# Optimization experiments

Measured on AMD Instinct MI355X. Metric: run time of the kernel, lower is better.

Reference implementation:

```python
import jax, jax.numpy as jnp
import numpy as np

N_HEAD = 32
HEAD_DIM = 32  # must equal N_HEAD due to the module's einsum index reuse
N_EMBD = N_HEAD * HEAD_DIM
VOCAB = 32000
B, T = 2, 64
TEMP_MIN = 0.1


def setup_inputs() -> dict:
    key = jax.random.key(0)
    ks = jax.random.split(key, 8)
    inv = 1.0 / np.sqrt(HEAD_DIM)
    return {
        "x": jax.random.normal(ks[0], (B, T, N_EMBD), dtype=jnp.float32),
        "vocab_emb": jax.random.normal(ks[1], (VOCAB, N_EMBD), dtype=jnp.float32) * 0.02,
        "W_ffn": jax.random.normal(ks[2], (HEAD_DIM, HEAD_DIM), dtype=jnp.float32) * inv,
        "b_ffn": jnp.zeros((HEAD_DIM,), dtype=jnp.float32),
        "temps": jnp.ones((N_HEAD,), dtype=jnp.float32),
        "W_ref": jax.random.normal(ks[3], (HEAD_DIM, HEAD_DIM), dtype=jnp.float32) * inv,
        "b_ref": jnp.zeros((HEAD_DIM,), dtype=jnp.float32),
        "W_gate": jax.random.normal(ks[4], (HEAD_DIM, HEAD_DIM), dtype=jnp.float32) * inv,
        "b_gate": jnp.zeros((HEAD_DIM,), dtype=jnp.float32),
    }


def reference(x, vocab_emb, W_ffn, b_ffn, temps, W_ref, b_ref, W_gate, b_gate):
    Bs, Ts, C = x.shape
    # per-head channel decomposition: (B*T, n_head, head_dim)
    xc = x.reshape(Bs * Ts, N_HEAD, HEAD_DIM)
    # channel_ffns: shared Linear over the head_dim axis (torch Linear: x @ W.T + b)
    ffn = jnp.einsum('bnh,dh->bnd', xc, W_ffn) + b_ffn
    # vocab channels: (n_head, vocab, head_dim)
    vc = vocab_emb.reshape(VOCAB, N_HEAD, HEAD_DIM).transpose(1, 0, 2)
    temps_c = jnp.clip(temps, TEMP_MIN, None)[None, :, None]

    def vocab_project(q):
        # faithful to torch: einsum('bnh,hvd->bnv') contracts q's head_dim
        # against vc's HEAD axis and sums over d as well (requires head_dim == n_head)
        logits = jnp.einsum('bnh,hvd->bnv', q, vc)
        w = jax.nn.softmax(logits / temps_c, axis=-1)  # (B*T, n_head, vocab)
        return jnp.einsum('bnv,hvd->bnh', w, vc)

    vocab_out = vocab_project(ffn)  # (B*T, n_head, head_dim)

    # refinement stage (use_vocab_refinement=True)
    refinement = jnp.tanh(jnp.einsum('bnh,dh->bnd', xc, W_ref) + b_ref)
    gate = jax.nn.sigmoid(jnp.einsum('bnh,dh->bnd', xc, W_gate) + b_gate)
    refined = vocab_out * (1.0 - gate) + refinement * gate
    vocab_out = vocab_project(refined)

    # dropout p=0 (eval) -> identity
    return vocab_out.reshape(Bs, Ts, C)
```

## Files before the change

kernel.cpp:

```cpp
#include <hip/hip_runtime.h>
#include <hip/hip_bf16.h>
#include <cstdint>

typedef unsigned int uint;
typedef unsigned short ushort_t;

typedef __attribute__((ext_vector_type(8))) short short8;
typedef __attribute__((ext_vector_type(4))) short short4_t;
typedef __attribute__((ext_vector_type(4))) float float4_t;

#define NEMBD 1024
#define VOCAB 32000
#define LOG2E 1.4426950408889634f

__device__ __forceinline__ ushort_t f2bf_rne(float f) {
    uint u = __float_as_uint(f);
    u += 0x7fffu + ((u >> 16) & 1u);
    return (ushort_t)(u >> 16);
}

__global__ void k_build_st(const float* __restrict__ ve, ushort_t* __restrict__ ST) {
    int v = blockIdx.x;
    int t = threadIdx.x;
    const float4* row = (const float4*)(ve + (size_t)v * NEMBD);
    float4 f = row[t];
    float s = f.x + f.y + f.z + f.w;
    s += __shfl_down(s, 4, 8);
    s += __shfl_down(s, 2, 8);
    s += __shfl_down(s, 1, 8);
    if ((t & 7) == 0) ST[v * 32 + (t >> 3)] = f2bf_rne(s);
}

__global__ void k_pack(const ushort_t* __restrict__ ST, ushort_t* __restrict__ SA,
                       ushort_t* __restrict__ S2) {
    int c = blockIdx.x;
    int t = threadIdx.x;
    if (t < 128) {
        int tile = t >> 6, lane = t & 63;
        int quad = lane >> 4, lo = lane & 15;
        uint4 d = *(const uint4*)(ST + ((size_t)(c * 32 + tile * 16 + lo)) * 32 + quad * 8);
        ((uint4*)SA)[c * 128 + t] = d;
    } else {
        int tt = t - 128;
        int f = tt >> 6, l = tt & 63;
        int quad = l >> 4, lo = l & 15;
        uint w[4];
        #pragma unroll
        for (int t2 = 0; t2 < 2; t2++) {
            #pragma unroll
            for (int jj = 0; jj < 2; jj++) {
                ushort_t v0 = ST[(c * 32 + t2 * 16 + quad * 4 + jj * 2 + 0) * 32 + f * 16 + lo];
                ushort_t v1 = ST[(c * 32 + t2 * 16 + quad * 4 + jj * 2 + 1) * 32 + f * 16 + lo];
                w[t2 * 2 + jj] = (uint)v0 | ((uint)v1 << 16);
            }
        }
        ((uint4*)S2)[c * 128 + tt] = make_uint4(w[0], w[1], w[2], w[3]);
    }
}

__global__ void k_q1(const float* __restrict__ x, const float* __restrict__ W,
                     const float* __restrict__ b, const float* __restrict__ temps,
                     ushort_t* __restrict__ q1) {
    int tid = blockIdx.x * 256 + threadIdx.x;
    int i = tid >> 5, d = tid & 31, n = i & 31;
    const float* xr = x + i * 32;
    float s = b[d];
    #pragma unroll
    for (int h = 0; h < 32; h++) s += xr[h] * W[d * 32 + h];
    q1[tid] = f2bf_rne(s * (LOG2E / fmaxf(temps[n], 0.1f)));
}

__launch_bounds__(256, 4)
__global__ void k_proj(const ushort_t* __restrict__ SA, const ushort_t* __restrict__ S2,
                       const ushort_t* __restrict__ q, float* __restrict__ pN,
                       float* __restrict__ pD) {
    int g = blockIdx.x >> 4, p = blockIdx.x & 15;
    int w = threadIdx.x >> 6, lane = threadIdx.x & 63;
    int quad = lane >> 4, lo = lane & 15;

    short8 qf[4];
    #pragma unroll
    for (int s = 0; s < 4; s++)
        qf[s] = *(const short8*)(q + ((g * 64 + s * 16 + lo) * 32 + quad * 8));

    float4_t pv0[4], pv1[4];
    float dsum[4];
    #pragma unroll
    for (int s = 0; s < 4; s++) {
        pv0[s] = (float4_t){0.f, 0.f, 0.f, 0.f};
        pv1[s] = (float4_t){0.f, 0.f, 0.f, 0.f};
        dsum[s] = 0.f;
    }
    const float4_t zero4 = (float4_t){0.f, 0.f, 0.f, 0.f};

    int start = (p * 125) >> 1, end = ((p + 1) * 125) >> 1;
    int k = start + w;
    const ushort_t* pa = SA + (size_t)k * 1024 + lane * 8;
    const ushort_t* pb = S2 + (size_t)k * 1024 + lane * 8;
    short8 a0n = *(const short8*)pa;
    short8 a1n = *(const short8*)(pa + 512);
    short8 b0n = *(const short8*)pb;
    short8 b1n = *(const short8*)(pb + 512);

    while (true) {
        short8 a0 = a0n, a1 = a1n, s0 = b0n, s1 = b1n;
        k += 4;
        bool more = (k < end);
        if (more) {
            pa += 4096; pb += 4096;
            a0n = *(const short8*)pa;
            a1n = *(const short8*)(pa + 512);
            b0n = *(const short8*)pb;
            b1n = *(const short8*)(pb + 512);
        }
        short4_t b00 = {s0[0], s0[1], s0[2], s0[3]};
        short4_t b01 = {s0[4], s0[5], s0[6], s0[7]};
        short4_t b10 = {s1[0], s1[1], s1[2], s1[3]};
        short4_t b11 = {s1[4], s1[5], s1[6], s1[7]};

        #pragma unroll
        for (int s = 0; s < 4; s++) {
            float4_t l0 = __builtin_amdgcn_mfma_f32_16x16x32_bf16(a0, qf[s], zero4, 0, 0, 0);
            float4_t l1 = __builtin_amdgcn_mfma_f32_16x16x32_bf16(a1, qf[s], zero4, 0, 0, 0);
            float e0 = __builtin_amdgcn_exp2f(l0[0]);
            float e1 = __builtin_amdgcn_exp2f(l0[1]);
            float e2 = __builtin_amdgcn_exp2f(l0[2]);
            float e3 = __builtin_amdgcn_exp2f(l0[3]);
            float f0 = __builtin_amdgcn_exp2f(l1[0]);
            float f1 = __builtin_amdgcn_exp2f(l1[1]);
            float f2 = __builtin_amdgcn_exp2f(l1[2]);
            float f3 = __builtin_amdgcn_exp2f(l1[3]);
            uint u0 = __builtin_amdgcn_perm(__float_as_uint(e1), __float_as_uint(e0), 0x07060302u);
            uint u1 = __builtin_amdgcn_perm(__float_as_uint(e3), __float_as_uint(e2), 0x07060302u);
            uint u2 = __builtin_amdgcn_perm(__float_as_uint(f1), __float_as_uint(f0), 0x07060302u);
            uint u3 = __builtin_amdgcn_perm(__float_as_uint(f3), __float_as_uint(f2), 0x07060302u);
            dsum[s] += __uint_as_float(u0 << 16) + __uint_as_float(u0 & 0xffff0000u)
                     + __uint_as_float(u1 << 16) + __uint_as_float(u1 & 0xffff0000u)
                     + __uint_as_float(u2 << 16) + __uint_as_float(u2 & 0xffff0000u)
                     + __uint_as_float(u3 << 16) + __uint_as_float(u3 & 0xffff0000u);
            union { uint u[2]; short4_t s4; } c0u, c1u;
            c0u.u[0] = u0; c0u.u[1] = u1;
            c1u.u[0] = u2; c1u.u[1] = u3;
            short4_t P0 = c0u.s4, P1 = c1u.s4;
            pv0[s] = __builtin_amdgcn_mfma_f32_16x16x16bf16_1k(P0, b00, pv0[s], 0, 0, 0);
            pv0[s] = __builtin_amdgcn_mfma_f32_16x16x16bf16_1k(P1, b01, pv0[s], 0, 0, 0);
            pv1[s] = __builtin_amdgcn_mfma_f32_16x16x16bf16_1k(P0, b10, pv1[s], 0, 0, 0);
            pv1[s] = __builtin_amdgcn_mfma_f32_16x16x16bf16_1k(P1, b11, pv1[s], 0, 0, 0);
        }
        if (!more) break;
    }

    #pragma unroll
    for (int s = 0; s < 4; s++) {
        dsum[s] += __shfl_xor(dsum[s], 16, 64);
        dsum[s] += __shfl_xor(dsum[s], 32, 64);
    }

    __shared__ float red[4][64][9];
    int gp = blockIdx.x;
    for (int s = 0; s < 4; s++) {
        #pragma unroll
        for (int r = 0; r < 4; r++) {
            red[w][lane][r]     = pv0[s][r];
            red[w][lane][4 + r] = pv1[s][r];
        }
        red[w][lane][8] = dsum[s];
        __syncthreads();
        if (w == 0) {
            #pragma unroll
            for (int r = 0; r < 4; r++) {
                float n0 = 0.f, n1 = 0.f;
                #pragma unroll
                for (int wv = 0; wv < 4; wv++) {
                    n0 += red[wv][lane][r];
                    n1 += red[wv][lane][4 + r];
                }
                int ql = s * 16 + quad * 4 + r;
                pN[((size_t)gp * 64 + ql) * 32 + lo]      = n0;
                pN[((size_t)gp * 64 + ql) * 32 + 16 + lo] = n1;
            }
            if (quad == 0) {
                float dd = red[0][lane][8] + red[1][lane][8]
                         + red[2][lane][8] + red[3][lane][8];
                pD[gp * 64 + s * 16 + lo] = dd;
            }
        }
        __syncthreads();
    }
}

__global__ void k_refine(const float* __restrict__ pN, const float* __restrict__ pD,
                         const float* __restrict__ x,
                         const float* __restrict__ Wr, const float* __restrict__ br,
                         const float* __restrict__ Wg, const float* __restrict__ bg,
                         const float* __restrict__ temps, ushort_t* __restrict__ q2) {
    int tid = blockIdx.x * 256 + threadIdx.x;
    int i = tid >> 5, h = tid & 31, n = i & 31;
    int g = i >> 6, ql = i & 63;
    float N = 0.f, D = 0.f;
    #pragma unroll
    for (int p = 0; p < 16; p++) {
        N += pN[((size_t)(g * 16 + p) * 64 + ql) * 32 + h];
        D += pD[(g * 16 + p) * 64 + ql];
    }
    float vo = N / D;
    const float* xr = x + i * 32;
    float sr = br[h], sg = bg[h];
    #pragma unroll
    for (int h2 = 0; h2 < 32; h2++) {
        sr += xr[h2] * Wr[h * 32 + h2];
        sg += xr[h2] * Wg[h * 32 + h2];
    }
    float ref  = tanhf(sr);
    float gate = 1.f / (1.f + __expf(-sg));
    float refined = vo * (1.f - gate) + ref * gate;
    q2[tid] = f2bf_rne(refined * (LOG2E / fmaxf(temps[n], 0.1f)));
}

__global__ void k_final(const float* __restrict__ pN, const float* __restrict__ pD,
                        float* __restrict__ out) {
    int tid = blockIdx.x * 256 + threadIdx.x;
    int i = tid >> 5, h = tid & 31;
    int g = i >> 6, ql = i & 63;
    float N = 0.f, D = 0.f;
    #pragma unroll
    for (int p = 0; p < 16; p++) {
        N += pN[((size_t)(g * 16 + p) * 64 + ql) * 32 + h];
        D += pD[(g * 16 + p) * 64 + ql];
    }
    out[tid] = N / D;
}

extern "C" void kernel_launch(void* const* d_in, const int* in_sizes, int n_in,
                              void* d_out, int out_size, void* d_ws, size_t ws_size,
                              hipStream_t stream) {
    const float* x     = (const float*)d_in[0];
    const float* ve    = (const float*)d_in[1];
    const float* Wf    = (const float*)d_in[2];
    const float* bfn   = (const float*)d_in[3];
    const float* temps = (const float*)d_in[4];
    const float* Wr    = (const float*)d_in[5];
    const float* br    = (const float*)d_in[6];
    const float* Wg    = (const float*)d_in[7];
    const float* bg    = (const float*)d_in[8];
    float* out = (float*)d_out;

    char* ws = (char*)d_ws;
    ushort_t* ST = (ushort_t*)ws;
    ushort_t* SA = (ushort_t*)(ws + 2048000);
    ushort_t* S2 = (ushort_t*)(ws + 4096000);
    ushort_t* q1 = (ushort_t*)(ws + 6144000);
    ushort_t* q2 = (ushort_t*)(ws + 6144000 + 262144);
    char* base = ws + 6144000 + 2 * 262144;
    float* pNa = (float*)base;
    float* pDa = (float*)(base + 8388608);
    float* pNb = (float*)(base + 8388608 + 262144);
    float* pDb = (float*)(base + 2 * 8388608 + 262144);

    k_build_st<<<dim3(VOCAB), dim3(256), 0, stream>>>(ve, ST);
    k_pack<<<dim3(1000), dim3(256), 0, stream>>>(ST, SA, S2);
    k_q1<<<dim3(512), dim3(256), 0, stream>>>(x, Wf, bfn, temps, q1);
    k_proj<<<dim3(1024), dim3(256), 0, stream>>>(SA, S2, q1, pNa, pDa);
    k_refine<<<dim3(512), dim3(256), 0, stream>>>(pNa, pDa, x, Wr, br, Wg, bg, temps, q2);
    k_proj<<<dim3(1024), dim3(256), 0, stream>>>(SA, S2, q2, pNb, pDb);
    k_final<<<dim3(512), dim3(256), 0, stream>>>(pNb, pDb, out);
}
```

Measured before the change: 271.4 us.

## Compute softmax denominators via MFMA with ones and double-buffer chunk loads

The per-lane scalar denominator sum (bf16 unpacking, adds, and cross-lane shuffles) is replaced by two extra MFMAs per step that multiply the packed probabilities by a vector of ones, so row sums land in accumulator registers. The load loop is restructured into an explicit two-buffer ping-pong, issuing the next chunk's global loads before computing the current one. This cuts VALU work and shuffles in the hot loop but adds MFMA work and more live registers. The shared-memory reduction now also sums the extra accumulator.

```diff
diff --git a/kernel.cpp b/kernel.cpp
--- a/kernel.cpp
+++ b/kernel.cpp
@@ -70,6 +70,41 @@
     q1[tid] = f2bf_rne(s * (LOG2E / fmaxf(temps[n], 0.1f)));
 }
 
+#define CHUNK_COMPUTE(A0, A1, S0, S1)                                              \
+    {                                                                              \
+        short4_t b00 = {(S0)[0], (S0)[1], (S0)[2], (S0)[3]};                       \
+        short4_t b01 = {(S0)[4], (S0)[5], (S0)[6], (S0)[7]};                       \
+        short4_t b10 = {(S1)[0], (S1)[1], (S1)[2], (S1)[3]};                       \
+        short4_t b11 = {(S1)[4], (S1)[5], (S1)[6], (S1)[7]};                       \
+        _Pragma("unroll")                                                          \
+        for (int s = 0; s < 4; s++) {                                              \
+            float4_t l0 = __builtin_amdgcn_mfma_f32_16x16x32_bf16(A0, qf[s], zero4, 0, 0, 0); \
+            float4_t l1 = __builtin_amdgcn_mfma_f32_16x16x32_bf16(A1, qf[s], zero4, 0, 0, 0); \
+            float e0 = __builtin_amdgcn_exp2f(l0[0]);                              \
+            float e1 = __builtin_amdgcn_exp2f(l0[1]);                              \
+            float e2 = __builtin_amdgcn_exp2f(l0[2]);                              \
+            float e3 = __builtin_amdgcn_exp2f(l0[3]);                              \
+            float f0 = __builtin_amdgcn_exp2f(l1[0]);                              \
+            float f1 = __builtin_amdgcn_exp2f(l1[1]);                              \
+            float f2 = __builtin_amdgcn_exp2f(l1[2]);                              \
+            float f3 = __builtin_amdgcn_exp2f(l1[3]);                              \
+            uint u0 = __builtin_amdgcn_perm(__float_as_uint(e1), __float_as_uint(e0), 0x07060302u); \
+            uint u1 = __builtin_amdgcn_perm(__float_as_uint(e3), __float_as_uint(e2), 0x07060302u); \
+            uint u2 = __builtin_amdgcn_perm(__float_as_uint(f1), __float_as_uint(f0), 0x07060302u); \
+            uint u3 = __builtin_amdgcn_perm(__float_as_uint(f3), __float_as_uint(f2), 0x07060302u); \
+            union { uint u[2]; short4_t s4; } c0u, c1u;                            \
+            c0u.u[0] = u0; c0u.u[1] = u1;                                          \
+            c1u.u[0] = u2; c1u.u[1] = u3;                                          \
+            short4_t P0 = c0u.s4, P1 = c1u.s4;                                     \
+            pv0[s] = __builtin_amdgcn_mfma_f32_16x16x16bf16_1k(P0, b00, pv0[s], 0, 0, 0); \
+            pv0[s] = __builtin_amdgcn_mfma_f32_16x16x16bf16_1k(P1, b01, pv0[s], 0, 0, 0); \
+            pv1[s] = __builtin_amdgcn_mfma_f32_16x16x16bf16_1k(P0, b10, pv1[s], 0, 0, 0); \
+            pv1[s] = __builtin_amdgcn_mfma_f32_16x16x16bf16_1k(P1, b11, pv1[s], 0, 0, 0); \
+            dq[s]  = __builtin_amdgcn_mfma_f32_16x16x16bf16_1k(P0, ones, dq[s], 0, 0, 0);  \
+            dq[s]  = __builtin_amdgcn_mfma_f32_16x16x16bf16_1k(P1, ones, dq[s], 0, 0, 0);  \
+        }                                                                          \
+    }
+
 __launch_bounds__(256, 4)
 __global__ void k_proj(const ushort_t* __restrict__ SA, const ushort_t* __restrict__ S2,
                        const ushort_t* __restrict__ q, float* __restrict__ pN,
@@ -83,106 +118,65 @@
     for (int s = 0; s < 4; s++)
         qf[s] = *(const short8*)(q + ((g * 64 + s * 16 + lo) * 32 + quad * 8));
 
-    float4_t pv0[4], pv1[4];
-    float dsum[4];
+    float4_t pv0[4], pv1[4], dq[4];
     #pragma unroll
     for (int s = 0; s < 4; s++) {
         pv0[s] = (float4_t){0.f, 0.f, 0.f, 0.f};
         pv1[s] = (float4_t){0.f, 0.f, 0.f, 0.f};
-        dsum[s] = 0.f;
+        dq[s]  = (float4_t){0.f, 0.f, 0.f, 0.f};
     }
     const float4_t zero4 = (float4_t){0.f, 0.f, 0.f, 0.f};
+    const short4_t ones = {(short)0x3F80, (short)0x3F80, (short)0x3F80, (short)0x3F80};
 
     int start = (p * 125) >> 1, end = ((p + 1) * 125) >> 1;
-    int k = start + w;
-    const ushort_t* pa = SA + (size_t)k * 1024 + lane * 8;
-    const ushort_t* pb = S2 + (size_t)k * 1024 + lane * 8;
-    short8 a0n = *(const short8*)pa;
-    short8 a1n = *(const short8*)(pa + 512);
-    short8 b0n = *(const short8*)pb;
-    short8 b1n = *(const short8*)(pb + 512);
-
+    int base_k = start + w;
+    int cnt = (end - base_k + 3) >> 2;
+    const ushort_t* pa = SA + (size_t)base_k * 1024 + lane * 8;
+    const ushort_t* pb = S2 + (size_t)base_k * 1024 + lane * 8;
+
+    short8 a0A = *(const short8*)pa, a1A = *(const short8*)(pa + 512);
+    short8 s0A = *(const short8*)pb, s1A = *(const short8*)(pb + 512);
+    pa += 4096; pb += 4096;
+    short8 a0B, a1B, s0B, s1B;
+
+    int i = 0;
     while (true) {
-        short8 a0 = a0n, a1 = a1n, s0 = b0n, s1 = b1n;
-        k += 4;
-        bool more = (k < end);
-        if (more) {
-            pa += 4096; pb += 4096;
-            a0n = *(const short8*)pa;
-            a1n = *(const short8*)(pa + 512);
-            b0n = *(const short8*)pb;
-            b1n = *(const short8*)(pb + 512);
-        }
-        short4_t b00 = {s0[0], s0[1], s0[2], s0[3]};
-        short4_t b01 = {s0[4], s0[5], s0[6], s0[7]};
-        short4_t b10 = {s1[0], s1[1], s1[2], s1[3]};
-        short4_t b11 = {s1[4], s1[5], s1[6], s1[7]};
-
-        #pragma unroll
-        for (int s = 0; s < 4; s++) {
-            float4_t l0 = __builtin_amdgcn_mfma_f32_16x16x32_bf16(a0, qf[s], zero4, 0, 0, 0);
-            float4_t l1 = __builtin_amdgcn_mfma_f32_16x16x32_bf16(a1, qf[s], zero4, 0, 0, 0);
-            float e0 = __builtin_amdgcn_exp2f(l0[0]);
-            float e1 = __builtin_amdgcn_exp2f(l0[1]);
-            float e2 = __builtin_amdgcn_exp2f(l0[2]);
-            float e3 = __builtin_amdgcn_exp2f(l0[3]);
-            float f0 = __builtin_amdgcn_exp2f(l1[0]);
-            float f1 = __builtin_amdgcn_exp2f(l1[1]);
-            float f2 = __builtin_amdgcn_exp2f(l1[2]);
-            float f3 = __builtin_amdgcn_exp2f(l1[3]);
-            uint u0 = __builtin_amdgcn_perm(__float_as_uint(e1), __float_as_uint(e0), 0x07060302u);
-            uint u1 = __builtin_amdgcn_perm(__float_as_uint(e3), __float_as_uint(e2), 0x07060302u);
-            uint u2 = __builtin_amdgcn_perm(__float_as_uint(f1), __float_as_uint(f0), 0x07060302u);
-            uint u3 = __builtin_amdgcn_perm(__float_as_uint(f3), __float_as_uint(f2), 0x07060302u);
-            dsum[s] += __uint_as_float(u0 << 16) + __uint_as_float(u0 & 0xffff0000u)
-                     + __uint_as_float(u1 << 16) + __uint_as_float(u1 & 0xffff0000u)
-                     + __uint_as_float(u2 << 16) + __uint_as_float(u2 & 0xffff0000u)
-                     + __uint_as_float(u3 << 16) + __uint_as_float(u3 & 0xffff0000u);
-            union { uint u[2]; short4_t s4; } c0u, c1u;
-            c0u.u[0] = u0; c0u.u[1] = u1;
-            c1u.u[0] = u2; c1u.u[1] = u3;
-            short4_t P0 = c0u.s4, P1 = c1u.s4;
-            pv0[s] = __builtin_amdgcn_mfma_f32_16x16x16bf16_1k(P0, b00, pv0[s], 0, 0, 0);
-            pv0[s] = __builtin_amdgcn_mfma_f32_16x16x16bf16_1k(P1, b01, pv0[s], 0, 0, 0);
-            pv1[s] = __builtin_amdgcn_mfma_f32_16x16x16bf16_1k(P0, b10, pv1[s], 0, 0, 0);
-            pv1[s] = __builtin_amdgcn_mfma_f32_16x16x16bf16_1k(P1, b11, pv1[s], 0, 0, 0);
-        }
-        if (!more) break;
-    }
-
-    #pragma unroll
-    for (int s = 0; s < 4; s++) {
-        dsum[s] += __shfl_xor(dsum[s], 16, 64);
-        dsum[s] += __shfl_xor(dsum[s], 32, 64);
-    }
-
-    __shared__ float red[4][64][9];
+        a0B = *(const short8*)pa; a1B = *(const short8*)(pa + 512);
+        s0B = *(const short8*)pb; s1B = *(const short8*)(pb + 512);
+        pa += 4096; pb += 4096;
+        CHUNK_COMPUTE(a0A, a1A, s0A, s1A);
+        if (++i >= cnt) break;
+        a0A = *(const short8*)pa; a1A = *(const short8*)(pa + 512);
+        s0A = *(const short8*)pb; s1A = *(const short8*)(pb + 512);
+        pa += 4096; pb += 4096;
+        CHUNK_COMPUTE(a0B, a1B, s0B, s1B);
+        if (++i >= cnt) break;
+    }
+
+    __shared__ float red[4][64][12];
     int gp = blockIdx.x;
     for (int s = 0; s < 4; s++) {
         #pragma unroll
         for (int r = 0; r < 4; r++) {
             red[w][lane][r]     = pv0[s][r];
             red[w][lane][4 + r] = pv1[s][r];
+            red[w][lane][8 + r] = dq[s][r];
         }
-        red[w][lane][8] = dsum[s];
         __syncthreads();
         if (w == 0) {
             #pragma unroll
             for (int r = 0; r < 4; r++) {
-                float n0 = 0.f, n1 = 0.f;
+                float n0 = 0.f, n1 = 0.f, dd = 0.f;
                 #pragma unroll
                 for (int wv = 0; wv < 4; wv++) {
                     n0 += red[wv][lane][r];
                     n1 += red[wv][lane][4 + r];
+                    dd += red[wv][lane][8 + r];
                 }
                 int ql = s * 16 + quad * 4 + r;
                 pN[((size_t)gp * 64 + ql) * 32 + lo]      = n0;
                 pN[((size_t)gp * 64 + ql) * 32 + 16 + lo] = n1;
-            }
-            if (quad == 0) {
-                float dd = red[0][lane][8] + red[1][lane][8]
-                         + red[2][lane][8] + red[3][lane][8];
-                pD[gp * 64 + s * 16 + lo] = dd;
+                if (lo == 0) pD[gp * 64 + ql] = dd;
             }
         }
         __syncthreads();
```

After: 299.9 us. 10.5% more time.
